# Kernel tuning notes

Hardware: AMD Instinct MI355X
Metric: run time of the kernel (lower is better)

## Reference

```python
import jax, jax.numpy as jnp
import numpy as np

B, S, E, H = 4, 4096, 1024, 128

def setup_inputs() -> dict:
    key = jax.random.key(0)
    kx, kk, kq, kv = jax.random.split(key, 4)
    x = jax.random.normal(kx, (B, S, E), dtype=jnp.float32)
    # torch nn.Linear weights are [out_features, in_features]
    Wk = jax.random.normal(kk, (H, E), dtype=jnp.float32) * (E ** -0.5)
    Wq = jax.random.normal(kq, (H, E), dtype=jnp.float32) * (E ** -0.5)
    Wv = jax.random.normal(kv, (H, E), dtype=jnp.float32) * (E ** -0.5)
    return {"x": x, "Wk": Wk, "Wq": Wq, "Wv": Wv}

def reference(x, Wk, Wq, Wv):
    # projections: y = x @ W.T  (bias-free nn.Linear)
    k = jnp.einsum('bse,he->bsh', x, Wk)
    q = jnp.einsum('bse,he->bsh', x, Wq)
    v = jnp.einsum('bse,he->bsh', x, Wv)
    emb = x.shape[-1]
    # scores scaled by embedding_size**-0.5 (as in the source, not head_size)
    scores = jnp.einsum('bqh,bkh->bqk', q, k) * (emb ** -0.5)  # [B,S,S]
    # causal mask: positions j > i get -inf
    i = jnp.arange(scores.shape[-2])[:, None]
    j = jnp.arange(scores.shape[-1])[None, :]
    scores = jnp.where(j > i, jnp.float32(-jnp.inf), scores)
    probs = jax.nn.softmax(scores, axis=-1)
    # dropout is identity in eval mode
    out = jnp.einsum('bqk,bkh->bqh', probs, v)  # [B,S,H]
    return out
```

## Files before the change

### kernel.cpp

```cpp
#include <hip/hip_runtime.h>

typedef short bf16x8 __attribute__((ext_vector_type(8)));
typedef float f32x4 __attribute__((ext_vector_type(4)));

#define MFMA16(a, b, c) __builtin_amdgcn_mfma_f32_16x16x32_bf16(a, b, c, 0, 0, 0)

constexpr int Bn = 4, Sn = 4096, En = 1024, Hn = 128;
constexpr float CSCALE = 1.44269504089f * 0.03125f;

__device__ inline int sb64(int qt) {
    int a = qt >> 4, r = qt & 15;
    return 8 * a * (a + 1) + r * (a + 1);
}
constexpr int SB = 160;
constexpr int SLOT_F = 8320;

__device__ inline unsigned short f2bf(float f) {
    unsigned int u = __builtin_bit_cast(unsigned int, f);
    u += 0x7fff + ((u >> 16) & 1);
    return (unsigned short)(u >> 16);
}

__device__ inline unsigned int pk2(float a, float b) {
    unsigned int ua = __builtin_bit_cast(unsigned int, a) + 0x8000u;
    unsigned int ub = __builtin_bit_cast(unsigned int, b) + 0x8000u;
    return __builtin_amdgcn_perm(ub, ua, 0x07060302u);
}

__device__ inline void gld16(const unsigned short* g, unsigned short* l) {
    __builtin_amdgcn_global_load_lds((const __attribute__((address_space(1))) void*)g,
                                     (__attribute__((address_space(3))) void*)l, 16, 0, 0);
}

__global__ __launch_bounds__(256) void prep_kernel(
    const float* __restrict__ Wk, const float* __restrict__ Wq, const float* __restrict__ Wv,
    unsigned short* __restrict__ wb, unsigned int* __restrict__ sched)
{
    int gy = blockIdx.x >> 5;
    const float* src = (gy == 0) ? Wq : (gy == 1) ? Wk : Wv;
    unsigned short* dst = wb + (size_t)gy * Hn * En;
    int t = (blockIdx.x & 31) * 256 + threadIdx.x;
    const float4* s4 = (const float4*)src;
    for (int i = 0; i < 4; ++i) {
        float4 v = s4[(size_t)t * 4 + i];
        uint2 w2 = { pk2(v.x, v.y), pk2(v.z, v.w) };
        *(uint2*)&dst[(size_t)t * 16 + i * 4] = w2;
    }
    if (blockIdx.x == 0) {
        const int bin = threadIdx.x;
        unsigned int it[4] = { 0xFFFFu, 0xFFFFu, 0xFFFFu, 0xFFFFu };
        auto fullItem = [](int k) -> unsigned int {
            int b = k / 100, j = k - 100 * b;
            int qt = 63, ch = 0;
            for (int q = 63; q >= 0; --q) {
                int f = (q + 1) >> 4;
                if (j < f) { qt = q; ch = j; break; }
                j -= f;
            }
            return (unsigned int)(qt | (ch << 6) | (b << 8));
        };
        auto remItem = [](int v, int i) -> unsigned int {
            int rep = i >> 2, b = i & 3;
            int qt = rep * 16 + v - 1, ch = rep;
            return (unsigned int)(qt | (ch << 6) | (b << 8));
        };
        if (bin < 128) {
            it[0] = fullItem(2 * bin);
            it[1] = fullItem(2 * bin + 1);
        } else if (bin < 240) {
            int t2 = bin - 128, v = 2 + (t2 >> 4), i = t2 & 15;
            it[0] = fullItem(256 + t2);
            it[1] = remItem(v, i);
            it[2] = remItem(17 - v, i);
        } else {
            int t2 = bin - 240;
            it[0] = fullItem(368 + 2 * t2);
            it[1] = fullItem(369 + 2 * t2);
            it[2] = remItem(1, t2);
        }
        for (int z = 0; z < 4; ++z) sched[z * 256 + bin] = it[z];
    }
}

__global__ __launch_bounds__(256, 3) void proj_kernel(
    const float* __restrict__ x, const unsigned short* __restrict__ wb,
    unsigned short* __restrict__ qb, unsigned short* __restrict__ kb,
    unsigned short* __restrict__ vbT)
{
    __shared__ __align__(16) unsigned short xs[2][64][64];
    __shared__ __align__(16) unsigned short wsm[2][128][64];

    const int gy = blockIdx.y;
    const unsigned short* wg = wb + (size_t)gy * Hn * En;

    const int m0 = blockIdx.x * 64;
    const int tid = threadIdx.x;
    const int lane = tid & 63, wave = tid >> 6;
    const int l15 = lane & 15, quad = lane >> 4;
    const int wm = (wave & 1) * 32;
    const int wn = (wave >> 1) * 64;

    f32x4 acc[2][4] = {};
    float4 xp[4];

    auto loadx = [&](int kc) {
        for (int p4 = 0; p4 < 4; ++p4) {
            int i = p4 * 256 + tid, row = i >> 4, c4 = (i & 15) * 4;
            xp[p4] = *(const float4*)&x[(size_t)(m0 + row) * En + kc * 64 + c4];
        }
    };
    auto writex = [&](int c) {
        for (int p4 = 0; p4 < 4; ++p4) {
            int i = p4 * 256 + tid, row = i >> 4, hc = i & 15;
            uint2 w2 = { pk2(xp[p4].x, xp[p4].y), pk2(xp[p4].z, xp[p4].w) };
            *(uint2*)((char*)&xs[c][0][0] + row * 128 + (((hc >> 1) ^ (row & 7)) << 4) + ((hc & 1) << 3)) = w2;
        }
    };
    auto issueW = [&](int kc, int c) {
        for (int j = 0; j < 4; ++j) {
            int seg = (wave * 4 + j) * 1024;
            int d = seg + (lane << 4);
            int row = d >> 7, chp = (d >> 4) & 7;
            gld16(wg + (size_t)row * En + kc * 64 + ((chp ^ (row & 7)) << 3),
                  (unsigned short*)((char*)&wsm[c][0][0] + seg));
        }
    };

    loadx(0);
    issueW(0, 0);
    writex(0);
    loadx(1);

    for (int kc = 0; kc < En / 64; ++kc) {
        const int c = kc & 1;
        __syncthreads();
        if (kc + 1 < En / 64) {
            issueW(kc + 1, c ^ 1);
            writex(c ^ 1);
            int kn = (kc + 2 < En / 64) ? kc + 2 : En / 64 - 1;
            loadx(kn);
        }
        bf16x8 xf[2][2], wf[4][2];
        for (int i = 0; i < 2; ++i)
            for (int kk = 0; kk < 2; ++kk) {
                int row = wm + i * 16 + l15;
                int chn = (kk * 4 + quad) ^ (row & 7);
                xf[i][kk] = *(const bf16x8*)((char*)&xs[c][0][0] + row * 128 + (chn << 4));
            }
        for (int j = 0; j < 4; ++j)
            for (int kk = 0; kk < 2; ++kk) {
                int row = wn + j * 16 + l15;
                int chn = (kk * 4 + quad) ^ (row & 7);
                wf[j][kk] = *(const bf16x8*)((char*)&wsm[c][0][0] + row * 128 + (chn << 4));
            }
        if (gy != 2) {
            for (int kk = 0; kk < 2; ++kk)
                for (int i = 0; i < 2; ++i)
                    for (int j = 0; j < 4; ++j)
                        acc[i][j] = MFMA16(xf[i][kk], wf[j][kk], acc[i][j]);
        } else {
            for (int kk = 0; kk < 2; ++kk)
                for (int i = 0; i < 2; ++i)
                    for (int j = 0; j < 4; ++j)
                        acc[i][j] = MFMA16(wf[j][kk], xf[i][kk], acc[i][j]);
        }
    }

    if (gy != 2) {
        unsigned short* ob = (gy == 0) ? qb : kb;
        const float osc = (gy == 0) ? CSCALE : 1.0f;
        for (int i = 0; i < 2; ++i) {
            int rowb = m0 + wm + i * 16 + quad * 4;
            for (int j = 0; j < 4; ++j) {
                int col = wn + j * 16 + l15;
                for (int r = 0; r < 4; ++r)
                    ob[(size_t)(rowb + r) * Hn + col] = f2bf(acc[i][j][r] * osc);
            }
        }
    } else {
        for (int j = 0; j < 4; ++j) {
            int hb = wn + j * 16 + quad * 4;
            for (int i = 0; i < 2; ++i) {
                int sp = m0 + wm + i * 16 + l15;
                int bb = sp >> 12, ss = sp & 4095;
                for (int r = 0; r < 4; ++r)
                    vbT[((size_t)(bb * 128 + hb + r)) * Sn + ss] = f2bf(acc[i][j][r]);
            }
        }
    }
}

__global__ __launch_bounds__(256, 3) void attn_kernel(
    const unsigned short* __restrict__ qb, const unsigned short* __restrict__ kb,
    const unsigned short* __restrict__ vbT, float* __restrict__ out,
    float* __restrict__ part, const unsigned int* __restrict__ sched)
{
    __shared__ unsigned short ks[64][132];
    __shared__ unsigned short vt[128][68];
    __shared__ unsigned short ps[4][16][72];

    const unsigned int wi = sched[blockIdx.x];
    if (wi == 0xFFFFu) return;
    const int qt = (int)(wi & 63u);
    const int ch = (int)((wi >> 6) & 3u);
    const int b  = (int)((wi >> 8) & 3u);
    const int T  = qt + 1;
    const int nch = (T + 15) >> 4;
    const int t0 = ch * 16;
    const int nloc = min(16, T - t0);
    const int q0 = qt * 64;

    const int tid = threadIdx.x;
    const int lane = tid & 63, wave = tid >> 6;
    const int l15 = lane & 15, quad = lane >> 4;

    const unsigned short* qg = qb + (size_t)(b * Sn + q0) * Hn;
    bf16x8 qf[4];
    for (int f = 0; f < 4; ++f)
        qf[f] = *(const bf16x8*)&qg[(wave * 16 + l15) * Hn + f * 32 + quad * 8];

    f32x4 o[8] = {};
    float m_r = -INFINITY, l_r = 0.f;

    const unsigned short* kg = kb + (size_t)b * Sn * Hn;
    const unsigned short* vg = vbT + (size_t)b * 128 * Sn;
    unsigned short* psrow = &ps[wave][l15][0];

    bf16x8 kreg[4], vreg[4];
    auto loadKV = [&](int gt) {
        int kt0 = gt * 64;
        for (int p4 = 0; p4 < 4; ++p4) {
            int i = p4 * 256 + tid;
            kreg[p4] = *(const bf16x8*)&kg[(size_t)(kt0 + (i >> 4)) * Hn + (i & 15) * 8];
            vreg[p4] = *(const bf16x8*)&vg[(size_t)(i >> 3) * Sn + kt0 + (i & 7) * 8];
        }
    };

    loadKV(t0);
    for (int tl = 0; tl < nloc; ++tl) {
        const int gt = t0 + tl;
        for (int p4 = 0; p4 < 4; ++p4) {
            int i = p4 * 256 + tid;
            *(bf16x8*)&ks[i >> 4][(i & 15) * 8] = kreg[p4];
            *(bf16x8*)&vt[i >> 3][(i & 7) * 8] = vreg[p4];
        }
        __syncthreads();
        if (tl + 1 < nloc) loadKV(gt + 1);

        float u[4][4];
        for (int nt = 0; nt < 4; ++nt) {
            f32x4 s = {};
            for (int kk = 0; kk < 4; ++kk) {
                bf16x8 kf = *(const bf16x8*)&ks[nt * 16 + l15][kk * 32 + quad * 8];
                s = MFMA16(kf, qf[kk], s);
            }
            for (int r = 0; r < 4; ++r) u[nt][r] = s[r];
        }
        if (gt == qt) {
            int qq = wave * 16 + l15;
            for (int nt = 0; nt < 4; ++nt)
                for (int r = 0; r < 4; ++r)
                    if (nt * 16 + quad * 4 + r > qq) u[nt][r] = -INFINITY;
        }
        float mx = -INFINITY;
        for (int nt = 0; nt < 4; ++nt)
            for (int r = 0; r < 4; ++r) mx = fmaxf(mx, u[nt][r]);
        mx = fmaxf(mx, __shfl_xor(mx, 16));
        mx = fmaxf(mx, __shfl_xor(mx, 32));
        float mn = fmaxf(m_r, mx);
        float alpha = exp2f(m_r - mn);
        m_r = mn;
        float sum = 0.f;
        for (int nt = 0; nt < 4; ++nt)
            for (int r = 0; r < 4; ++r) {
                float pv = exp2f(u[nt][r] - mn);
                u[nt][r] = pv;
                sum += pv;
            }
        sum += __shfl_xor(sum, 16);
        sum += __shfl_xor(sum, 32);
        l_r = l_r * alpha + sum;

        for (int nt = 0; nt < 4; ++nt) {
            uint2 w2 = { pk2(u[nt][0], u[nt][1]), pk2(u[nt][2], u[nt][3]) };
            *(uint2*)&psrow[nt * 16 + quad * 4] = w2;
        }
        for (int t = 0; t < 8; ++t) o[t] *= alpha;

        for (int k2 = 0; k2 < 2; ++k2) {
            bf16x8 pf = *(const bf16x8*)&psrow[k2 * 32 + quad * 8];
            for (int t = 0; t < 8; ++t) {
                bf16x8 vf = *(const bf16x8*)&vt[t * 16 + l15][k2 * 32 + quad * 8];
                o[t] = MFMA16(vf, pf, o[t]);
            }
        }
        __syncthreads();
    }

    if (nch == 1) {
        float inv = 1.0f / l_r;
        float* og = out + (size_t)(b * Sn + q0 + wave * 16 + l15) * Hn;
        for (int t = 0; t < 8; ++t) {
            float4 st = { o[t][0] * inv, o[t][1] * inv, o[t][2] * inv, o[t][3] * inv };
            *(float4*)&og[t * 16 + quad * 4] = st;
        }
    } else {
        float* P = part + (size_t)(b * SB + sb64(qt) + ch) * SLOT_F;
        int q = wave * 16 + l15;
        for (int t = 0; t < 8; ++t) {
            float4 st = { o[t][0], o[t][1], o[t][2], o[t][3] };
            *(float4*)&P[q * 128 + t * 16 + quad * 4] = st;
        }
        if (quad == 0) {
            P[8192 + q] = m_r;
            P[8256 + q] = l_r;
        }
    }
}

__global__ __launch_bounds__(256) void merge_kernel(
    const float* __restrict__ part, float* __restrict__ out)
{
    const int qt = 16 + blockIdx.x;
    const int b = blockIdx.y;
    const int nch = (qt + 16) >> 4;
    const float* P0 = part + (size_t)(b * SB + sb64(qt)) * SLOT_F;
    const int q = threadIdx.x >> 2;
    const int h0 = (threadIdx.x & 3) * 32;

    float m[4], w[4];
    float M = -INFINITY;
    for (int c = 0; c < nch; ++c) {
        m[c] = P0[(size_t)c * SLOT_F + 8192 + q];
        M = fmaxf(M, m[c]);
    }
    float L = 0.f;
    for (int c = 0; c < nch; ++c) {
        w[c] = exp2f(m[c] - M);
        L += w[c] * P0[(size_t)c * SLOT_F + 8256 + q];
    }
    float inv = 1.0f / L;

    float acc[32] = {};
    for (int c = 0; c < nch; ++c) {
        const float* Pq = P0 + (size_t)c * SLOT_F + q * 128 + h0;
        for (int j = 0; j < 8; ++j) {
            float4 v = *(const float4*)&Pq[j * 4];
            acc[j * 4 + 0] += w[c] * v.x;
            acc[j * 4 + 1] += w[c] * v.y;
            acc[j * 4 + 2] += w[c] * v.z;
            acc[j * 4 + 3] += w[c] * v.w;
        }
    }
    float* og = out + (size_t)(b * Sn + qt * 64 + q) * Hn + h0;
    for (int j = 0; j < 8; ++j) {
        float4 st = { acc[j * 4 + 0] * inv, acc[j * 4 + 1] * inv,
                      acc[j * 4 + 2] * inv, acc[j * 4 + 3] * inv };
        *(float4*)&og[j * 4] = st;
    }
}

extern "C" void kernel_launch(void* const* d_in, const int* in_sizes, int n_in,
                              void* d_out, int out_size, void* d_ws, size_t ws_size,
                              hipStream_t stream)
{
    const float* x  = (const float*)d_in[0];
    const float* Wk = (const float*)d_in[1];
    const float* Wq = (const float*)d_in[2];
    const float* Wv = (const float*)d_in[3];
    float* out = (float*)d_out;

    unsigned short* qbuf  = (unsigned short*)d_ws;
    unsigned short* kbuf  = qbuf + (size_t)Bn * Sn * Hn;
    unsigned short* vbufT = kbuf + (size_t)Bn * Sn * Hn;
    unsigned short* wb    = vbufT + (size_t)Bn * Sn * Hn;
    float* part = (float*)(wb + (size_t)3 * Hn * En);
    unsigned int* sched = (unsigned int*)part;

    prep_kernel<<<96, 256, 0, stream>>>(Wk, Wq, Wv, wb, sched);
    proj_kernel<<<dim3(Bn * Sn / 64, 3), 256, 0, stream>>>(x, wb, qbuf, kbuf, vbufT);
    attn_kernel<<<1024, 256, 0, stream>>>(qbuf, kbuf, vbufT, out, part, sched);
    merge_kernel<<<dim3(48, Bn), 256, 0, stream>>>(part, out);
}
```

Measured before the change: 174.4 us.

## Fuse Q/K/V projections into one block per row tile to share x loads

The projection kernel now computes all three Q, K and V outputs in a single 512-thread block per 64-row tile, instead of launching a separate grid slice for each. Each x tile is read from global memory and converted to bf16 once rather than three times. Each of the 8 waves covers 48 output columns across the concatenated 384-wide weight, so LDS for weights triples and occupancy drops to 2 blocks of 512 threads. The grid shrinks to 256 blocks. The V output is now written transposed as packed 4-element vectors, using the standard MFMA operand order rather than the swapped one.

```diff
diff --git a/kernel.cpp b/kernel.cpp
--- a/kernel.cpp
+++ b/kernel.cpp
@@ -82,46 +82,42 @@
     }
 }
 
-__global__ __launch_bounds__(256, 3) void proj_kernel(
+__global__ __launch_bounds__(512, 2) void proj_kernel(
     const float* __restrict__ x, const unsigned short* __restrict__ wb,
     unsigned short* __restrict__ qb, unsigned short* __restrict__ kb,
     unsigned short* __restrict__ vbT)
 {
     __shared__ __align__(16) unsigned short xs[2][64][64];
-    __shared__ __align__(16) unsigned short wsm[2][128][64];
-
-    const int gy = blockIdx.y;
-    const unsigned short* wg = wb + (size_t)gy * Hn * En;
+    __shared__ __align__(16) unsigned short wsm[2][384][64];
 
     const int m0 = blockIdx.x * 64;
     const int tid = threadIdx.x;
     const int lane = tid & 63, wave = tid >> 6;
     const int l15 = lane & 15, quad = lane >> 4;
-    const int wm = (wave & 1) * 32;
-    const int wn = (wave >> 1) * 64;
-
-    f32x4 acc[2][4] = {};
-    float4 xp[4];
+    const int wn = wave * 48;
+
+    f32x4 acc[4][3] = {};
+    float4 xp[2];
 
     auto loadx = [&](int kc) {
-        for (int p4 = 0; p4 < 4; ++p4) {
-            int i = p4 * 256 + tid, row = i >> 4, c4 = (i & 15) * 4;
-            xp[p4] = *(const float4*)&x[(size_t)(m0 + row) * En + kc * 64 + c4];
+        for (int p2 = 0; p2 < 2; ++p2) {
+            int i = p2 * 512 + tid, row = i >> 4, c4 = (i & 15) * 4;
+            xp[p2] = *(const float4*)&x[(size_t)(m0 + row) * En + kc * 64 + c4];
         }
     };
     auto writex = [&](int c) {
-        for (int p4 = 0; p4 < 4; ++p4) {
-            int i = p4 * 256 + tid, row = i >> 4, hc = i & 15;
-            uint2 w2 = { pk2(xp[p4].x, xp[p4].y), pk2(xp[p4].z, xp[p4].w) };
+        for (int p2 = 0; p2 < 2; ++p2) {
+            int i = p2 * 512 + tid, row = i >> 4, hc = i & 15;
+            uint2 w2 = { pk2(xp[p2].x, xp[p2].y), pk2(xp[p2].z, xp[p2].w) };
             *(uint2*)((char*)&xs[c][0][0] + row * 128 + (((hc >> 1) ^ (row & 7)) << 4) + ((hc & 1) << 3)) = w2;
         }
     };
     auto issueW = [&](int kc, int c) {
-        for (int j = 0; j < 4; ++j) {
-            int seg = (wave * 4 + j) * 1024;
+        for (int j = 0; j < 6; ++j) {
+            int seg = (wave * 6 + j) * 1024;
             int d = seg + (lane << 4);
             int row = d >> 7, chp = (d >> 4) & 7;
-            gld16(wg + (size_t)row * En + kc * 64 + ((chp ^ (row & 7)) << 3),
+            gld16(wb + (size_t)row * En + kc * 64 + ((chp ^ (row & 7)) << 3),
                   (unsigned short*)((char*)&wsm[c][0][0] + seg));
         }
     };
@@ -140,51 +136,40 @@
             int kn = (kc + 2 < En / 64) ? kc + 2 : En / 64 - 1;
             loadx(kn);
         }
-        bf16x8 xf[2][2], wf[4][2];
-        for (int i = 0; i < 2; ++i)
+        bf16x8 xf[4][2], wf[3][2];
+        for (int i = 0; i < 4; ++i)
             for (int kk = 0; kk < 2; ++kk) {
-                int row = wm + i * 16 + l15;
+                int row = i * 16 + l15;
                 int chn = (kk * 4 + quad) ^ (row & 7);
                 xf[i][kk] = *(const bf16x8*)((char*)&xs[c][0][0] + row * 128 + (chn << 4));
             }
-        for (int j = 0; j < 4; ++j)
+        for (int j = 0; j < 3; ++j)
             for (int kk = 0; kk < 2; ++kk) {
                 int row = wn + j * 16 + l15;
                 int chn = (kk * 4 + quad) ^ (row & 7);
                 wf[j][kk] = *(const bf16x8*)((char*)&wsm[c][0][0] + row * 128 + (chn << 4));
             }
-        if (gy != 2) {
-            for (int kk = 0; kk < 2; ++kk)
-                for (int i = 0; i < 2; ++i)
-                    for (int j = 0; j < 4; ++j)
-                        acc[i][j] = MFMA16(xf[i][kk], wf[j][kk], acc[i][j]);
-        } else {
-            for (int kk = 0; kk < 2; ++kk)
-                for (int i = 0; i < 2; ++i)
-                    for (int j = 0; j < 4; ++j)
-                        acc[i][j] = MFMA16(wf[j][kk], xf[i][kk], acc[i][j]);
-        }
-    }
-
-    if (gy != 2) {
-        unsigned short* ob = (gy == 0) ? qb : kb;
-        const float osc = (gy == 0) ? CSCALE : 1.0f;
-        for (int i = 0; i < 2; ++i) {
-            int rowb = m0 + wm + i * 16 + quad * 4;
-            for (int j = 0; j < 4; ++j) {
-                int col = wn + j * 16 + l15;
+        for (int kk = 0; kk < 2; ++kk)
+            for (int i = 0; i < 4; ++i)
+                for (int j = 0; j < 3; ++j)
+                    acc[i][j] = MFMA16(xf[i][kk], wf[j][kk], acc[i][j]);
+    }
+
+    for (int i = 0; i < 4; ++i) {
+        int rowb = m0 + i * 16 + quad * 4;
+        for (int j = 0; j < 3; ++j) {
+            int gcol = wn + j * 16 + l15;
+            int gy = gcol >> 7, col = gcol & 127;
+            if (gy == 0) {
                 for (int r = 0; r < 4; ++r)
-                    ob[(size_t)(rowb + r) * Hn + col] = f2bf(acc[i][j][r] * osc);
-            }
-        }
-    } else {
-        for (int j = 0; j < 4; ++j) {
-            int hb = wn + j * 16 + quad * 4;
-            for (int i = 0; i < 2; ++i) {
-                int sp = m0 + wm + i * 16 + l15;
-                int bb = sp >> 12, ss = sp & 4095;
+                    qb[(size_t)(rowb + r) * Hn + col] = f2bf(acc[i][j][r] * CSCALE);
+            } else if (gy == 1) {
                 for (int r = 0; r < 4; ++r)
-                    vbT[((size_t)(bb * 128 + hb + r)) * Sn + ss] = f2bf(acc[i][j][r]);
+                    kb[(size_t)(rowb + r) * Hn + col] = f2bf(acc[i][j][r]);
+            } else {
+                int bb = rowb >> 12, ss = rowb & 4095;
+                uint2 w2 = { pk2(acc[i][j][0], acc[i][j][1]), pk2(acc[i][j][2], acc[i][j][3]) };
+                *(uint2*)&vbT[((size_t)(bb * 128 + col)) * Sn + ss] = w2;
             }
         }
     }
@@ -378,7 +363,7 @@
     unsigned int* sched = (unsigned int*)part;
 
     prep_kernel<<<96, 256, 0, stream>>>(Wk, Wq, Wv, wb, sched);
-    proj_kernel<<<dim3(Bn * Sn / 64, 3), 256, 0, stream>>>(x, wb, qbuf, kbuf, vbufT);
+    proj_kernel<<<256, 512, 0, stream>>>(x, wb, qbuf, kbuf, vbufT);
     attn_kernel<<<1024, 256, 0, stream>>>(qbuf, kbuf, vbufT, out, part, sched);
     merge_kernel<<<dim3(48, Bn), 256, 0, stream>>>(part, out);
 }
```

Result: no change. 176.4 us (+1.1%).
